# Kernel tuning notes

Measured on AMD Instinct MI355X. Metric: run time of the kernel, lower is better.

## Reference

```python
import jax, jax.numpy as jnp
import numpy as np

# Dimensions (match init_kwargs / input_specs)
B, CIN, COUT = 4, 8, 32
HIN, WIN = 721, 1440      # input (nlat, nlon)
HOUT, WOUT = 361, 720     # output (nlat, nlon)
K = 9                     # morlet basis: kernel_shape[0]*kernel_shape[1]
NNZ = 32                  # nonzeros per (basis fn, output-lat) row of sparse psi
PSCALE = WIN // WOUT      # longitudinal downsampling factor (must be integer)


def setup_inputs() -> dict:
    key = jax.random.key(0)
    k1, k2, k3, k4, k5 = jax.random.split(key, 5)
    x = jax.random.normal(k1, (B, CIN, HIN, WIN), jnp.float32)
    # Localized sparse support: input lat rows near the matching output lat
    # (emulates the theta_cutoff neighborhood of the precomputed DISCO tensor).
    base_row = jnp.round(jnp.arange(HOUT) * (HIN - 1) / (HOUT - 1)).astype(jnp.int32)
    drow = jax.random.randint(k2, (K, HOUT, NNZ), -2, 3)
    rows = jnp.clip(base_row[None, :, None] + drow, 0, HIN - 1)
    # small longitudinal offsets; the contraction shifts them over all output lons
    cols = jax.random.randint(k3, (K, HOUT, NNZ), 0, 16)
    psi_idx = (rows * WIN + cols).astype(jnp.int32)          # [K, HOUT, NNZ]
    psi_vals = jax.random.normal(k4, (K, HOUT, NNZ), jnp.float32) / NNZ
    weight = jax.random.normal(k5, (COUT, CIN, K), jnp.float32) / np.sqrt(CIN * K)
    return {"x": x, "psi_idx": psi_idx, "psi_vals": psi_vals, "weight": weight}


def _disco_conv(x, psi_idx, psi_vals, weight):
    # DISCO S2 contraction (dense math of torch_harmonics _disco_s2_contraction):
    #   out[b,o,xo,po] = sum_{c,k} weight[o,c,k] * y[b,c,k,xo,po]
    Bv, C, Hin, Win = x.shape
    rows = psi_idx // Win               # [K, Hout, NNZ]
    cols = psi_idx % Win
    x_flat = x.reshape(Bv, C, Hin * Win)

    def step(_, po):
        cols_p = (cols + po * PSCALE) % Win
        idx = rows * Win + cols_p                        # [K,Hout,NNZ]
        xg = x_flat[:, :, idx]                           # [B,C,K,Hout,NNZ] gather
        y_po = jnp.einsum('bckxn,kxn->bckx', xg, psi_vals)
        return None, y_po

    _, y = jax.lax.scan(step, None, jnp.arange(WOUT))    # [Wout,B,C,K,Hout]
    out = jnp.einsum('pbckx,ock->boxp', y, weight)       # [B,Cout,Hout,Wout]
    return out


def reference(x, psi_idx, psi_vals, weight):
    # The wrapper only casts to float32 around the conv; inputs are already fp32.
    return _disco_conv(x.astype(jnp.float32), psi_idx, psi_vals, weight)
```

## Files before the change

### kernel.cpp

```cpp
#include <hip/hip_runtime.h>
#include <hip/hip_bf16.h>

#define HIN   721
#define WIN   1440
#define HOUT_ 361
#define WOUT_ 720
#define NB    4
#define CIN_  8
#define COUT_ 32
#define KT    9
#define NNZ_  32

typedef short  bsh8   __attribute__((ext_vector_type(8)));
typedef float  f32x16 __attribute__((ext_vector_type(16)));
typedef unsigned int u32x4 __attribute__((ext_vector_type(4)));

static __device__ __forceinline__ unsigned short f2bf(float f) {
  unsigned u = __builtin_bit_cast(unsigned, f);
  u += 0x7fffu + ((u >> 16) & 1u);
  return (unsigned short)(u >> 16);
}

static __device__ __forceinline__ unsigned pack2(float a, float b) {
  __hip_bfloat162 h = __float22bfloat162_rn(make_float2(a, b));
  unsigned u; __builtin_memcpy(&u, &h, 4);
  return u;
}

__global__ __launch_bounds__(256, 3) void coeff_kernel(
    const int*   __restrict__ psi_idx,
    const float* __restrict__ psi_vals,
    const float* __restrict__ weight,
    unsigned short* __restrict__ Cg)
{
  __shared__ unsigned short Cl16[256 * 83];
  __shared__ float S[KT][80];

  const int x = blockIdx.x, tid = threadIdx.x;

  for (int i = tid; i < KT * 80; i += 256) ((float*)S)[i] = 0.f;
  __syncthreads();

  for (int i = tid; i < KT * NNZ_; i += 256) {
    int k = i >> 5, n = i & 31;
    int gi  = (k * HOUT_ + x) * NNZ_ + n;
    int idx = psi_idx[gi];
    int r   = idx / WIN;
    int col = idx - r * WIN;
    int s   = r - 2 * x + 2;
    int slot = (s * 2 + (col & 1)) * 8 + (col >> 1);
    atomicAdd(&S[k][slot], psi_vals[gi]);
  }

  float w[KT];
  #pragma unroll
  for (int k = 0; k < KT; ++k) w[k] = weight[tid * KT + k];
  __syncthreads();

  {
    unsigned short* seg = &Cl16[tid * 83];
    #pragma unroll
    for (int slot = 0; slot < 80; ++slot) {
      float acc = 0.f;
      #pragma unroll
      for (int k = 0; k < KT; ++k) acc += w[k] * S[k][slot];
      seg[slot] = f2bf(acc);
    }
  }
  __syncthreads();

  for (int chunk = tid; chunk < 8 * 10 * 32; chunk += 256) {
    int j   = chunk / 320;
    int rem = chunk - j * 320;
    int qb  = rem >> 5, o = rem & 31;
    u32x4 pack;
    #pragma unroll
    for (int h = 0; h < 4; ++h) {
      int q0 = qb * 8 + 2 * h;
      int c0 = q0 / 10, ql0 = q0 - c0 * 10;
      int q1 = q0 + 1;
      int c1 = q1 / 10, ql1 = q1 - c1 * 10;
      unsigned lo = Cl16[(o * CIN_ + c0) * 83 + ql0 * 8 + j];
      unsigned hi = Cl16[(o * CIN_ + c1) * 83 + ql1 * 8 + j];
      pack[h] = lo | (hi << 16);
    }
    *(u32x4*)&Cg[((size_t)x * 2560 + (size_t)((j * 10 + qb) * 32 + o)) * 8] = pack;
  }
}

#define PB   256
#define ROWS 264
#define RST  176

__global__ __launch_bounds__(256, 3) void disco_main_kernel(
    const float* __restrict__ x,
    const unsigned short* __restrict__ Cg,
    float* __restrict__ out)
{
  __shared__ __align__(16) unsigned char Ut[ROWS * RST];

  const int g   = blockIdx.x;
  const int xcd = g & 7, lin = g >> 3;
  const int swz = (xcd < 4) ? xcd * 542 + lin : 4 * 542 + (xcd - 4) * 541 + lin;
  const int xo  = swz / 12;
  const int rem = swz - xo * 12;
  const int pt  = rem % 3;
  const int b   = rem / 3;
  const int p0  = pt * PB;
  const int tid = threadIdx.x;

  const int lane = tid & 63;
  const int wv   = tid >> 6;
  const int half = lane >> 5;
  const int l31  = lane & 31;
  const int wbase = wv * 64;

  const unsigned short* cgx = Cg + (size_t)xo * 2560 * 8
                                 + (size_t)(half * 32 + l31) * 8;

  bsh8 afr[2][5];
  #pragma unroll
  for (int kb = 0; kb < 5; ++kb) afr[0][kb] = *(const bsh8*)&cgx[kb * 512];
  #pragma unroll
  for (int kb = 0; kb < 5; ++kb) afr[1][kb] = *(const bsh8*)&cgx[2560 + kb * 512];

  const float* xb = x + (size_t)b * (CIN_ * HIN * WIN);

  int rr[5];
  #pragma unroll
  for (int s = 0; s < 5; ++s) {
    int r = 2 * xo + s - 2;
    rr[s] = r < 0 ? 0 : (r > HIN - 1 ? HIN - 1 : r);
  }

  #pragma unroll
  for (int bp = 0; bp < 2; ++bp) {
    float4 v0[4], v1[4];
    const int uA = tid + (2 * bp) * 256, uB = uA + 256;
    const int chA = uA / 132, rpA = uA - chA * 132;
    const int chB = uB / 132, rpB = uB - chB * 132;
    int cwA = p0 + 2 * rpA; if (cwA >= WOUT_) cwA -= WOUT_;
    int cwB = p0 + 2 * rpB; if (cwB >= WOUT_) cwB -= WOUT_;
    #pragma unroll
    for (int m = 0; m < 4; ++m) {
      int qpA = 4 * chA + m, cA = (qpA * 205) >> 10, sA = qpA - cA * 5;
      v0[m] = *(const float4*)&xb[(size_t)(cA * HIN + rr[sA]) * WIN + 2 * cwA];
      int qpB = 4 * chB + m, cB = (qpB * 205) >> 10, sB = qpB - cB * 5;
      v1[m] = *(const float4*)&xb[(size_t)(cB * HIN + rr[sB]) * WIN + 2 * cwB];
    }
    u32x4 lo, hi;
    #pragma unroll
    for (int m = 0; m < 4; ++m) { lo[m] = pack2(v0[m].x, v0[m].y); hi[m] = pack2(v0[m].z, v0[m].w); }
    int byte0 = (2 * rpA) * RST + chA * 16;
    *(u32x4*)&Ut[byte0]       = lo;
    *(u32x4*)&Ut[byte0 + RST] = hi;
    #pragma unroll
    for (int m = 0; m < 4; ++m) { lo[m] = pack2(v1[m].x, v1[m].y); hi[m] = pack2(v1[m].z, v1[m].w); }
    byte0 = (2 * rpB) * RST + chB * 16;
    *(u32x4*)&Ut[byte0]       = lo;
    *(u32x4*)&Ut[byte0 + RST] = hi;
  }
  {
    const int uA = tid + 1024;
    const int chA = uA / 132, rpA = uA - chA * 132;
    int cwA = p0 + 2 * rpA; if (cwA >= WOUT_) cwA -= WOUT_;
    float4 v0[4], v1[4];
    int chB = 0, rpB = 0;
    const bool tail = tid < 40;
    if (tail) {
      const int uB = tid + 1280;
      chB = uB / 132; rpB = uB - chB * 132;
    }
    int cwB = p0 + 2 * rpB; if (cwB >= WOUT_) cwB -= WOUT_;
    #pragma unroll
    for (int m = 0; m < 4; ++m) {
      int qpA = 4 * chA + m, cA = (qpA * 205) >> 10, sA = qpA - cA * 5;
      v0[m] = *(const float4*)&xb[(size_t)(cA * HIN + rr[sA]) * WIN + 2 * cwA];
    }
    if (tail) {
      #pragma unroll
      for (int m = 0; m < 4; ++m) {
        int qpB = 4 * chB + m, cB = (qpB * 205) >> 10, sB = qpB - cB * 5;
        v1[m] = *(const float4*)&xb[(size_t)(cB * HIN + rr[sB]) * WIN + 2 * cwB];
      }
    }
    u32x4 lo, hi;
    #pragma unroll
    for (int m = 0; m < 4; ++m) { lo[m] = pack2(v0[m].x, v0[m].y); hi[m] = pack2(v0[m].z, v0[m].w); }
    int byte0 = (2 * rpA) * RST + chA * 16;
    *(u32x4*)&Ut[byte0]       = lo;
    *(u32x4*)&Ut[byte0 + RST] = hi;
    if (tail) {
      #pragma unroll
      for (int m = 0; m < 4; ++m) { lo[m] = pack2(v1[m].x, v1[m].y); hi[m] = pack2(v1[m].z, v1[m].w); }
      byte0 = (2 * rpB) * RST + chB * 16;
      *(u32x4*)&Ut[byte0]       = lo;
      *(u32x4*)&Ut[byte0 + RST] = hi;
    }
  }
  __syncthreads();

  f32x16 acc0 = {};
  f32x16 acc1 = {};

  bsh8 bc0[5], bc1[5];
  {
    const int rb0 = (wbase + l31) * RST;
    const int rb1 = rb0 + 32 * RST;
    #pragma unroll
    for (int kb = 0; kb < 5; ++kb) {
      const int cho = (2 * kb + half) * 16;
      bc0[kb] = *(const bsh8*)&Ut[rb0 + cho];
      bc1[kb] = *(const bsh8*)&Ut[rb1 + cho];
    }
  }

  #pragma unroll
  for (int j = 0; j < 8; ++j) {
    bsh8 bn0[5], bn1[5];
    if (j < 7) {
      const int rb0 = (wbase + l31 + j + 1) * RST;
      const int rb1 = rb0 + 32 * RST;
      #pragma unroll
      for (int kb = 0; kb < 5; ++kb) {
        const int cho = (2 * kb + half) * 16;
        bn0[kb] = *(const bsh8*)&Ut[rb0 + cho];
        bn1[kb] = *(const bsh8*)&Ut[rb1 + cho];
      }
    }
    __builtin_amdgcn_s_setprio(1);
    #pragma unroll
    for (int kb = 0; kb < 5; ++kb) {
      acc0 = __builtin_amdgcn_mfma_f32_32x32x16_bf16(afr[j & 1][kb], bc0[kb], acc0, 0, 0, 0);
      acc1 = __builtin_amdgcn_mfma_f32_32x32x16_bf16(afr[j & 1][kb], bc1[kb], acc1, 0, 0, 0);
    }
    __builtin_amdgcn_s_setprio(0);
    if (j < 6) {
      #pragma unroll
      for (int kb = 0; kb < 5; ++kb)
        afr[j & 1][kb] = *(const bsh8*)&cgx[(j + 2) * 2560 + kb * 512];
    }
    #pragma unroll
    for (int kb = 0; kb < 5; ++kb) { bc0[kb] = bn0[kb]; bc1[kb] = bn1[kb]; }
  }

  const int p = p0 + wbase + l31;
  #pragma unroll
  for (int r = 0; r < 16; ++r) {
    int o = (r & 3) + 8 * (r >> 2) + 4 * half;
    size_t base = ((size_t)(b * COUT_ + o) * HOUT_ + xo) * WOUT_;
    if (p < WOUT_)
      __builtin_nontemporal_store(acc0[r], &out[base + p]);
    if (p + 32 < WOUT_)
      __builtin_nontemporal_store(acc1[r], &out[base + p + 32]);
  }
}

extern "C" void kernel_launch(void* const* d_in, const int* in_sizes, int n_in,
                              void* d_out, int out_size, void* d_ws, size_t ws_size,
                              hipStream_t stream) {
  const float* x        = (const float*)d_in[0];
  const int*   psi_idx  = (const int*)d_in[1];
  const float* psi_vals = (const float*)d_in[2];
  const float* weight   = (const float*)d_in[3];
  float* out = (float*)d_out;
  unsigned short* Cg = (unsigned short*)d_ws;

  coeff_kernel<<<dim3(HOUT_), 256, 0, stream>>>(psi_idx, psi_vals, weight, Cg);
  disco_main_kernel<<<dim3(3 * NB * HOUT_), 256, 0, stream>>>(x, Cg, out);
}
```

Measured before the change: 86.26 us.

## Make each wave stage its own overlapping LDS row slice and drop the block barrier

The input staging is re-partitioned so that each wave loads and bf16-packs exactly the 72 shared-memory rows its own MFMA loop reads. Because no wave depends on rows written by another wave, the block-wide __syncthreads before the compute loop is removed and waves can start their matrix ops independently. The cost is about 8 redundant rows per wave, which means extra global loads. Adjacent waves also write identical values to the same LDS locations, a race that is harmless only because the values match.

```diff
diff --git a/kernel.cpp b/kernel.cpp
--- a/kernel.cpp
+++ b/kernel.cpp
@@ -133,72 +133,86 @@
     rr[s] = r < 0 ? 0 : (r > HIN - 1 ? HIN - 1 : r);
   }
 
-  #pragma unroll
-  for (int bp = 0; bp < 2; ++bp) {
-    float4 v0[4], v1[4];
-    const int uA = tid + (2 * bp) * 256, uB = uA + 256;
-    const int chA = uA / 132, rpA = uA - chA * 132;
-    const int chB = uB / 132, rpB = uB - chB * 132;
-    int cwA = p0 + 2 * rpA; if (cwA >= WOUT_) cwA -= WOUT_;
-    int cwB = p0 + 2 * rpB; if (cwB >= WOUT_) cwB -= WOUT_;
-    #pragma unroll
-    for (int m = 0; m < 4; ++m) {
-      int qpA = 4 * chA + m, cA = (qpA * 205) >> 10, sA = qpA - cA * 5;
-      v0[m] = *(const float4*)&xb[(size_t)(cA * HIN + rr[sA]) * WIN + 2 * cwA];
-      int qpB = 4 * chB + m, cB = (qpB * 205) >> 10, sB = qpB - cB * 5;
-      v1[m] = *(const float4*)&xb[(size_t)(cB * HIN + rr[sB]) * WIN + 2 * cwB];
-    }
-    u32x4 lo, hi;
-    #pragma unroll
-    for (int m = 0; m < 4; ++m) { lo[m] = pack2(v0[m].x, v0[m].y); hi[m] = pack2(v0[m].z, v0[m].w); }
-    int byte0 = (2 * rpA) * RST + chA * 16;
-    *(u32x4*)&Ut[byte0]       = lo;
-    *(u32x4*)&Ut[byte0 + RST] = hi;
-    #pragma unroll
-    for (int m = 0; m < 4; ++m) { lo[m] = pack2(v1[m].x, v1[m].y); hi[m] = pack2(v1[m].z, v1[m].w); }
-    byte0 = (2 * rpB) * RST + chB * 16;
-    *(u32x4*)&Ut[byte0]       = lo;
-    *(u32x4*)&Ut[byte0 + RST] = hi;
-  }
-  {
-    const int uA = tid + 1024;
-    const int chA = uA / 132, rpA = uA - chA * 132;
-    int cwA = p0 + 2 * rpA; if (cwA >= WOUT_) cwA -= WOUT_;
-    float4 v0[4], v1[4];
-    int chB = 0, rpB = 0;
-    const bool tail = tid < 40;
-    if (tail) {
-      const int uB = tid + 1280;
-      chB = uB / 132; rpB = uB - chB * 132;
-    }
-    int cwB = p0 + 2 * rpB; if (cwB >= WOUT_) cwB -= WOUT_;
-    #pragma unroll
-    for (int m = 0; m < 4; ++m) {
-      int qpA = 4 * chA + m, cA = (qpA * 205) >> 10, sA = qpA - cA * 5;
-      v0[m] = *(const float4*)&xb[(size_t)(cA * HIN + rr[sA]) * WIN + 2 * cwA];
-    }
-    if (tail) {
+  {
+    float4 v[3][4];
+    #pragma unroll
+    for (int k = 0; k < 3; ++k) {
+      const int i  = lane + k * 64;
+      const int ch = i / 36, rp = i - ch * 36;
+      const int t  = wbase + 2 * rp;
+      int cw = p0 + t; if (cw >= WOUT_) cw -= WOUT_;
       #pragma unroll
       for (int m = 0; m < 4; ++m) {
-        int qpB = 4 * chB + m, cB = (qpB * 205) >> 10, sB = qpB - cB * 5;
-        v1[m] = *(const float4*)&xb[(size_t)(cB * HIN + rr[sB]) * WIN + 2 * cwB];
-      }
-    }
-    u32x4 lo, hi;
-    #pragma unroll
-    for (int m = 0; m < 4; ++m) { lo[m] = pack2(v0[m].x, v0[m].y); hi[m] = pack2(v0[m].z, v0[m].w); }
-    int byte0 = (2 * rpA) * RST + chA * 16;
-    *(u32x4*)&Ut[byte0]       = lo;
-    *(u32x4*)&Ut[byte0 + RST] = hi;
-    if (tail) {
-      #pragma unroll
-      for (int m = 0; m < 4; ++m) { lo[m] = pack2(v1[m].x, v1[m].y); hi[m] = pack2(v1[m].z, v1[m].w); }
-      byte0 = (2 * rpB) * RST + chB * 16;
+        int qp = 4 * ch + m, c = (qp * 205) >> 10, s = qp - c * 5;
+        v[k][m] = *(const float4*)&xb[(size_t)(c * HIN + rr[s]) * WIN + 2 * cw];
+      }
+    }
+    #pragma unroll
+    for (int k = 0; k < 3; ++k) {
+      const int i  = lane + k * 64;
+      const int ch = i / 36, rp = i - ch * 36;
+      const int t  = wbase + 2 * rp;
+      u32x4 lo, hi;
+      #pragma unroll
+      for (int m = 0; m < 4; ++m) { lo[m] = pack2(v[k][m].x, v[k][m].y);
+                                    hi[m] = pack2(v[k][m].z, v[k][m].w); }
+      const int byte0 = t * RST + ch * 16;
       *(u32x4*)&Ut[byte0]       = lo;
       *(u32x4*)&Ut[byte0 + RST] = hi;
     }
   }
-  __syncthreads();
+  {
+    float4 v[2][4], vt[4];
+    const bool tl = lane < 40;
+    #pragma unroll
+    for (int k = 0; k < 2; ++k) {
+      const int i  = lane + (3 + k) * 64;
+      const int ch = i / 36, rp = i - ch * 36;
+      const int t  = wbase + 2 * rp;
+      int cw = p0 + t; if (cw >= WOUT_) cw -= WOUT_;
+      #pragma unroll
+      for (int m = 0; m < 4; ++m) {
+        int qp = 4 * ch + m, c = (qp * 205) >> 10, s = qp - c * 5;
+        v[k][m] = *(const float4*)&xb[(size_t)(c * HIN + rr[s]) * WIN + 2 * cw];
+      }
+    }
+    if (tl) {
+      const int i  = 320 + lane;
+      const int ch = i / 36, rp = i - ch * 36;
+      const int t  = wbase + 2 * rp;
+      int cw = p0 + t; if (cw >= WOUT_) cw -= WOUT_;
+      #pragma unroll
+      for (int m = 0; m < 4; ++m) {
+        int qp = 4 * ch + m, c = (qp * 205) >> 10, s = qp - c * 5;
+        vt[m] = *(const float4*)&xb[(size_t)(c * HIN + rr[s]) * WIN + 2 * cw];
+      }
+    }
+    #pragma unroll
+    for (int k = 0; k < 2; ++k) {
+      const int i  = lane + (3 + k) * 64;
+      const int ch = i / 36, rp = i - ch * 36;
+      const int t  = wbase + 2 * rp;
+      u32x4 lo, hi;
+      #pragma unroll
+      for (int m = 0; m < 4; ++m) { lo[m] = pack2(v[k][m].x, v[k][m].y);
+                                    hi[m] = pack2(v[k][m].z, v[k][m].w); }
+      const int byte0 = t * RST + ch * 16;
+      *(u32x4*)&Ut[byte0]       = lo;
+      *(u32x4*)&Ut[byte0 + RST] = hi;
+    }
+    if (tl) {
+      const int i  = 320 + lane;
+      const int ch = i / 36, rp = i - ch * 36;
+      const int t  = wbase + 2 * rp;
+      u32x4 lo, hi;
+      #pragma unroll
+      for (int m = 0; m < 4; ++m) { lo[m] = pack2(vt[m].x, vt[m].y);
+                                    hi[m] = pack2(vt[m].z, vt[m].w); }
+      const int byte0 = t * RST + ch * 16;
+      *(u32x4*)&Ut[byte0]       = lo;
+      *(u32x4*)&Ut[byte0 + RST] = hi;
+    }
+  }
 
   f32x16 acc0 = {};
   f32x16 acc1 = {};
```

Result: slower. 89.38 us (+3.6%).
